# Kernel optimization log

Hardware: AMD Instinct MI355X
Metric: run time of the kernel (lower is better)

## Reference

```python
import jax, jax.numpy as jnp
import numpy as np

# Spiking time schedule: B_n = (1+0.5)*X_n = 1500 per spiking layer (X_n=1000),
# chained via set_params: layer k has t_min = 1500*k, t_max = 1500*(k+1).
B_N = 1500.0


def _region_idx(H, W):
    # 0=center, 1=TL, 2=top, 3=TR, 4=right, 5=BR, 6=bottom, 7=BL, 8=left
    r = np.zeros((H, W), np.int32)
    r[0, :] = 2; r[-1, :] = 6; r[:, 0] = 8; r[:, -1] = 4
    r[0, 0] = 1; r[0, -1] = 3; r[-1, -1] = 5; r[-1, 0] = 7
    return jnp.asarray(r)


def _im2col3(x, t_min):
    # x: [B,H,W,C] -> patches [B,H,W,9*C]; 'same' pad with value t_min
    B, H, W, C = x.shape
    xp = jnp.pad(x, ((0, 0), (1, 1), (1, 1), (0, 0)), constant_values=t_min)
    cols = [xp[:, dy:dy + H, dx:dx + W, :] for dy in range(3) for dx in range(3)]
    return jnp.concatenate(cols, axis=-1)


def _spiking_conv(x, Wk, D, t_min, t_max):
    # ti = (tj - t_min) @ W + (t_max - t_min - D_region) + t_min, clamped at t_max
    p = _im2col3(x, t_min)                       # [B,H,W,9C]
    lin = jnp.einsum('bhwk,kf->bhwf', p - t_min, Wk)
    Dmap = D[_region_idx(x.shape[1], x.shape[2])]  # [H,W,F] border-aware thresholds
    return jnp.minimum(lin + (t_max - Dmap), t_max)


def _spiking_dense(x, Wk, D, t_min, t_max):
    return jnp.minimum((x - t_min) @ Wk + (t_max - D), t_max)


def _pool2(x):
    B, H, W, C = x.shape
    return x.reshape(B, H // 2, 2, W // 2, 2, C).max(axis=(2, 4))


def _forward(x, Wc1, Dc1, Wc2, Dc2, Wc3, Dc3, Wc4, Dc4, Wd1, Dd1, Wout, Dout):
    x = _spiking_conv(x, Wc1, Dc1, 0.0, 1500.0)
    x = _spiking_conv(x, Wc2, Dc2, 1500.0, 3000.0)
    x = _pool2(x)
    x = _spiking_conv(x, Wc3, Dc3, 3000.0, 4500.0)
    x = _spiking_conv(x, Wc4, Dc4, 4500.0, 6000.0)
    x = _pool2(x)
    x = x.reshape(x.shape[0], -1)                 # [B, 16*16*128]
    x = _spiking_dense(x, Wd1, Dd1, 6000.0, 7500.0)
    # output layer: alpha*(t_min - t_min_prev) + (t_min - tj)@W == D_i + (t_min - tj)@W
    return Dout + (7500.0 - x) @ Wout


def setup_inputs() -> dict:
    key = jax.random.key(0)
    ks = jax.random.split(key, 14)
    B, H, C0 = 32, 64, 1

    def w(k, fan_in, fan_out):
        return (jax.random.normal(k, (fan_in, fan_out), jnp.float32)
                / np.float32(np.sqrt(fan_in)))

    def d(k, shape):
        return jax.random.uniform(k, shape, jnp.float32) * 10.0

    return {
        'x': jax.random.uniform(ks[0], (B, H, H, C0), jnp.float32),
        'Wc1': w(ks[1], 9 * C0, 64),    'Dc1': d(ks[2], (9, 64)),
        'Wc2': w(ks[3], 9 * 64, 64),    'Dc2': d(ks[4], (9, 64)),
        'Wc3': w(ks[5], 9 * 64, 128),   'Dc3': d(ks[6], (9, 128)),
        'Wc4': w(ks[7], 9 * 128, 128),  'Dc4': d(ks[8], (9, 128)),
        'Wd1': w(ks[9], 16 * 16 * 128, 256), 'Dd1': d(ks[10], (256,)),
        'Wout': w(ks[11], 256, 10),     'Dout': d(ks[12], (10,)),
    }


def reference(x, Wc1, Dc1, Wc2, Dc2, Wc3, Dc3, Wc4, Dc4, Wd1, Dd1, Wout, Dout):
    return _forward(x, Wc1, Dc1, Wc2, Dc2, Wc3, Dc3, Wc4, Dc4, Wd1, Dd1, Wout, Dout)
```

## Files before the change

kernel.cpp:

```cpp
#include <hip/hip_runtime.h>
#include <hip/hip_bf16.h>

#define DEVINL __device__ __forceinline__

typedef __attribute__((ext_vector_type(8)))  short short8;
typedef __attribute__((ext_vector_type(4)))  float float4v;

DEVINL float bf2f(unsigned short u) { return __uint_as_float(((unsigned)u) << 16); }
DEVINL unsigned short f2bf(float f) {
  unsigned u = __float_as_uint(f);
  unsigned r = u + 0x7FFFu + ((u >> 16) & 1u);
  return (unsigned short)(r >> 16);
}
DEVINL unsigned f2bf_u(float f) { return (unsigned)f2bf(f); }

DEVINL int region_of(int h, int w, int n) {
  if (h == 0)     return (w == 0) ? 1 : ((w == n-1) ? 3 : 2);
  if (h == n-1)   return (w == 0) ? 7 : ((w == n-1) ? 5 : 6);
  return (w == 0) ? 8 : ((w == n-1) ? 4 : 0);
}

__global__ void sentinel_k(float* out, float v) {
  int t = blockIdx.x*64 + threadIdx.x;
  if (t < 320) out[t] = v;
}

__global__ void wtrans_all(const float* __restrict__ W1, const float* __restrict__ W2,
                           const float* __restrict__ W3, const float* __restrict__ W4,
                           unsigned short* __restrict__ T1, unsigned short* __restrict__ T2,
                           unsigned short* __restrict__ T3, unsigned short* __restrict__ T4)
{
  int y = blockIdx.y;
  int i = blockIdx.x*256 + threadIdx.x;
  if (y == 3) {
    if (i >= 256) return;
    int lane = i & 63, nt = i >> 6;
    int lm = lane & 15, q = lane >> 4;
    int f = nt*16 + lm;
    unsigned short v[8] = {0,0,0,0,0,0,0,0};
    if ((q & 1) == 0) {
      #pragma unroll
      for (int j = 0; j < 8; j++) v[j] = f2bf(W1[j*64 + f]);
    } else {
      v[0] = f2bf(W1[8*64 + f]);
    }
    ushort4* qq = (ushort4*)&T1[(size_t)i * 8];
    qq[0] = make_ushort4(v[0], v[1], v[2], v[3]);
    qq[1] = make_ushort4(v[4], v[5], v[6], v[7]);
    return;
  }
  const float* W = (y == 0) ? W2 : (y == 1) ? W3 : W4;
  unsigned short* T = (y == 0) ? T2 : (y == 1) ? T3 : T4;
  int Ksteps = (y == 2) ? 36 : 18;
  int NT = (y == 0) ? 4 : 8;
  int F  = (y == 0) ? 64 : 128;
  if (i >= Ksteps*NT*64) return;
  int lane = i & 63, nt = (i >> 6) % NT, kstep = i / (64*NT);
  int f = nt*16 + (lane & 15);
  int kbase = kstep*32 + (lane >> 4)*8;
  unsigned short v[8];
  #pragma unroll
  for (int j = 0; j < 8; j++) v[j] = f2bf(W[(kbase + j)*F + f]);
  ushort4* q = (ushort4*)&T[(size_t)i * 8];
  q[0] = make_ushort4(v[0], v[1], v[2], v[3]);
  q[1] = make_ushort4(v[4], v[5], v[6], v[7]);
}

__global__ __launch_bounds__(256, 4) void conv12_k(const float* __restrict__ x,
    const unsigned short* __restrict__ Wt1, const float* __restrict__ Df1,
    const unsigned short* __restrict__ Wt, const float* __restrict__ Df2,
    unsigned short* __restrict__ out)
{
  constexpr int Cpad = 72;
  __shared__ __align__(16) unsigned short u[4*66*Cpad];
  __shared__ float xs[6][66];

  int b = blockIdx.y, hp = blockIdx.x, t = threadIdx.x;
  int h0 = hp * 2;

  for (int idx = t; idx < 6*66; idx += 256) {
    int r = idx / 66, wc = idx % 66;
    int hh = h0 - 2 + r, w = wc - 1;
    float v = 0.f;
    if (hh >= 0 && hh < 64 && w >= 0 && w < 64) v = x[(b*64 + hh)*64 + w];
    xs[r][wc] = v;
  }
  {
    int r = t >> 6, c = (t >> 5) & 1, f2 = (t & 31) * 2;
    *(unsigned*)&u[(r*66 + (c ? 65 : 0))*Cpad + f2] = 0u;
  }
  __syncthreads();

  int lane = t & 63, wave = t >> 6;
  int quad = lane >> 4, lm = lane & 15;
  union ABu { float4 f4; short8 v; };
  union AW  { unsigned w32[4]; short8 v; };

  {
    short8 b1[4];
    #pragma unroll
    for (int nt = 0; nt < 4; nt++) {
      ABu tmp;
      tmp.f4 = *(const float4*)&Wt1[(size_t)((nt*64) + lane)*8];
      b1[nt] = tmp.v;
    }
    int wl = wave*16 + lm;
    bool fullq = ((quad & 1) == 0);
    bool hiq   = (quad < 2);

    for (int r = 0; r < 4; r++) {
      int hh = h0 - 1 + r;
      if (hh >= 0 && hh < 64) {
        float v[9];
        #pragma unroll
        for (int k = 0; k < 9; k++) v[k] = xs[r + k/3][wl + k%3];
        unsigned hb[9], lb[9];
        #pragma unroll
        for (int k = 0; k < 9; k++) {
          hb[k] = f2bf_u(v[k]);
          lb[k] = f2bf_u(v[k] - bf2f((unsigned short)hb[k]));
        }
        unsigned Hp[4], Lp[4];
        #pragma unroll
        for (int j = 0; j < 4; j++) {
          Hp[j] = hb[2*j] | (hb[2*j+1] << 16);
          Lp[j] = lb[2*j] | (lb[2*j+1] << 16);
        }
        AW a;
        a.w32[0] = fullq ? (hiq ? Hp[0] : Lp[0]) : (hiq ? hb[8] : lb[8]);
        a.w32[1] = fullq ? (hiq ? Hp[1] : Lp[1]) : 0u;
        a.w32[2] = fullq ? (hiq ? Hp[2] : Lp[2]) : 0u;
        a.w32[3] = fullq ? (hiq ? Hp[3] : Lp[3]) : 0u;

        float4v acc1[4];
        #pragma unroll
        for (int nt = 0; nt < 4; nt++)
          acc1[nt] = __builtin_amdgcn_mfma_f32_16x16x32_bf16(a.v, b1[nt],
                       (float4v){0.f,0.f,0.f,0.f}, 0, 0, 0);

        #pragma unroll
        for (int nt = 0; nt < 4; nt++) {
          int f = nt*16 + lm;
          #pragma unroll
          for (int reg = 0; reg < 4; reg++) {
            int w = wave*16 + quad*4 + reg;
            float val = fminf(acc1[nt][reg] - Df1[region_of(hh, w, 64)*64 + f], 0.f);
            u[(r*66 + (w+1))*Cpad + f] = f2bf(val);
          }
        }
      } else {
        #pragma unroll
        for (int nt = 0; nt < 4; nt++)
          #pragma unroll
          for (int reg = 0; reg < 4; reg++)
            u[(r*66 + (wave*16 + quad*4 + reg + 1))*Cpad + nt*16 + lm] = 0;
      }
    }
  }
  __syncthreads();

  int wm = wave >> 1, wn = wave & 1;

  float4v acc[2][2][2];
  #pragma unroll
  for (int hi = 0; hi < 2; hi++)
    #pragma unroll
    for (int m = 0; m < 2; m++)
      #pragma unroll
      for (int n = 0; n < 2; n++)
        acc[hi][m][n] = (float4v){0.f, 0.f, 0.f, 0.f};

  #pragma unroll
  for (int dy = 0; dy < 3; dy++)
  #pragma unroll
  for (int dx = 0; dx < 3; dx++)
  #pragma unroll
  for (int c0 = 0; c0 < 64; c0 += 32) {
    int kstep = (dy*3 + dx)*2 + (c0 >> 5);
    ABu bfr[2];
    #pragma unroll
    for (int n = 0; n < 2; n++)
      bfr[n].f4 = *(const float4*)&Wt[(size_t)((kstep*4 + wn*2 + n)*64 + lane)*8];
    #pragma unroll
    for (int hi = 0; hi < 2; hi++) {
      ABu afr[2];
      #pragma unroll
      for (int m = 0; m < 2; m++)
        afr[m].f4 = *(const float4*)&u[((hi+dy)*66 + ((wm*2 + m)*16 + lm + dx))*Cpad + c0 + quad*8];
      #pragma unroll
      for (int n = 0; n < 2; n++)
        #pragma unroll
        for (int m = 0; m < 2; m++)
          acc[hi][m][n] = __builtin_amdgcn_mfma_f32_16x16x32_bf16(afr[m].v, bfr[n].v, acc[hi][m][n], 0, 0, 0);
    }
  }

  #pragma unroll
  for (int m = 0; m < 2; m++)
    #pragma unroll
    for (int n = 0; n < 2; n++) {
      int mm = wm*2 + m;
      int f = (wn*2 + n)*16 + lm;
      #pragma unroll
      for (int rp = 0; rp < 2; rp++) {
        float mx = -1e30f;
        #pragma unroll
        for (int hi = 0; hi < 2; hi++)
          #pragma unroll
          for (int rr = 0; rr < 2; rr++) {
            int h = h0 + hi, w = mm*16 + quad*4 + 2*rp + rr;
            float v = fminf(acc[hi][m][n][2*rp+rr] - Df2[region_of(h, w, 64)*64 + f], 0.f);
            mx = fmaxf(mx, v);
          }
        int wp = mm*8 + quad*2 + rp;
        out[(((size_t)b*32 + hp)*32 + wp)*64 + f] = f2bf(mx);
      }
    }
}

template<int C, int F, int N, bool POOL, int FS, int MINW>
__global__ __launch_bounds__(256, MINW) void conv_mfma(
    const unsigned short* __restrict__ U, const unsigned short* __restrict__ Wt,
    const float* __restrict__ Df, unsigned short* __restrict__ out)
{
  constexpr int RC   = POOL ? 2 : 1;
  constexpr int ROWS = RC + 2;
  constexpr int Cpad = C + 8;
  constexpr int NT = F / 16;
  constexpr int MT = N / 16;
  constexpr int NTE = NT / FS;
  constexpr int MW = MT;
  constexpr int NW = NTE / 4;

  __shared__ __align__(16) unsigned short lds[ROWS*(N+2)*Cpad];

  int bx = blockIdx.x, b = blockIdx.y, t = threadIdx.x;
  int hp = bx / FS, fs = bx % FS;
  int h0 = hp * RC;

  const int stage16 = ROWS*(N+2)*(C/8);
  #pragma unroll 4
  for (int i = t; i < stage16; i += 256) {
    int c8 = i % (C/8), wc = (i/(C/8)) % (N+2), r = i/((C/8)*(N+2));
    int hh = h0 - 1 + r, w = wc - 1;
    float4 v = make_float4(0.f,0.f,0.f,0.f);
    if (hh >= 0 && hh < N && w >= 0 && w < N)
      v = *(const float4*)&U[(((size_t)b*N + hh)*N + w)*C + c8*8];
    *(float4*)&lds[(r*(N+2) + wc)*Cpad + c8*8] = v;
  }
  __syncthreads();

  int lane = t & 63, wave = t >> 6;
  int wn = wave;
  int quad = lane >> 4, lm = lane & 15;

  union ABu { float4 f4; short8 v; };

  float4v acc[RC][MW][NW];
  #pragma unroll
  for (int hi = 0; hi < RC; hi++)
    #pragma unroll
    for (int m = 0; m < MW; m++)
      #pragma unroll
      for (int n = 0; n < NW; n++)
        acc[hi][m][n] = (float4v){0.f, 0.f, 0.f, 0.f};

  #pragma unroll
  for (int dy = 0; dy < 3; dy++)
  #pragma unroll
  for (int dx = 0; dx < 3; dx++)
  #pragma unroll
  for (int c0 = 0; c0 < C; c0 += 32) {
    int kstep = (dy*3 + dx)*(C/32) + (c0 >> 5);
    ABu bfr[NW];
    #pragma unroll
    for (int n = 0; n < NW; n++)
      bfr[n].f4 = *(const float4*)&Wt[(size_t)((kstep*NT + fs*NTE + wn*NW + n)*64 + lane)*8];
    #pragma unroll
    for (int hi = 0; hi < RC; hi++) {
      ABu afr[MW];
      #pragma unroll
      for (int m = 0; m < MW; m++)
        afr[m].f4 = *(const float4*)&lds[((hi+dy)*(N+2) + (m*16 + lm + dx))*Cpad + c0 + quad*8];
      #pragma unroll
      for (int n = 0; n < NW; n++)
        #pragma unroll
        for (int m = 0; m < MW; m++)
          acc[hi][m][n] = __builtin_amdgcn_mfma_f32_16x16x32_bf16(afr[m].v, bfr[n].v, acc[hi][m][n], 0, 0, 0);
    }
  }

  if constexpr (POOL) {
    constexpr int M2 = N/2;
    #pragma unroll
    for (int m = 0; m < MW; m++)
      #pragma unroll
      for (int n = 0; n < NW; n++) {
        int f = (fs*NTE + wn*NW + n)*16 + lm;
        #pragma unroll
        for (int rp = 0; rp < 2; rp++) {
          float mx = -1e30f;
          #pragma unroll
          for (int hi = 0; hi < 2; hi++)
            #pragma unroll
            for (int rr = 0; rr < 2; rr++) {
              int h = h0 + hi, w = m*16 + quad*4 + 2*rp + rr;
              float v = fminf(acc[hi][m][n][2*rp+rr] - Df[region_of(h, w, N)*F + f], 0.f);
              mx = fmaxf(mx, v);
            }
          int wp = m*8 + quad*2 + rp;
          out[(((size_t)b*M2 + hp)*M2 + wp)*F + f] = f2bf(mx);
        }
      }
  } else {
    int h = h0;
    #pragma unroll
    for (int m = 0; m < MW; m++)
      #pragma unroll
      for (int n = 0; n < NW; n++) {
        int f = (fs*NTE + wn*NW + n)*16 + lm;
        #pragma unroll
        for (int r = 0; r < 4; r++) {
          int w = m*16 + quad*4 + r;
          int reg = region_of(h, w, N);
          float v = fminf(acc[0][m][n][r] - Df[reg*F + f], 0.f);
          out[(((size_t)b*N + h)*N + w)*F + f] = f2bf(v);
        }
      }
  }
}

__global__ __launch_bounds__(256, 2) void conv4_k(
    const unsigned short* __restrict__ U, const unsigned short* __restrict__ Wt,
    const float* __restrict__ Df, unsigned short* __restrict__ out)
{
  constexpr int C = 128, Cpad = 136, N = 32;
  __shared__ __align__(16) unsigned short lds[3*34*Cpad];

  int b = blockIdx.y, hp = blockIdx.x, t = threadIdx.x;
  int h0 = hp * 2;

  const int stage16 = 3*34*(C/8);
  #pragma unroll 4
  for (int i = t; i < stage16; i += 256) {
    int c8 = i % 16, wc = (i/16) % 34, r = i/(16*34);
    int hh = h0 - 1 + r, w = wc - 1;
    float4 v = make_float4(0.f,0.f,0.f,0.f);
    if (hh >= 0 && hh < N && w >= 0 && w < N)
      v = *(const float4*)&U[(((size_t)b*N + hh)*N + w)*C + c8*8];
    *(float4*)&lds[(r*34 + wc)*Cpad + c8*8] = v;
  }
  __syncthreads();

  int lane = t & 63, wave = t >> 6;
  int wn = wave, quad = lane >> 4, lm = lane & 15;
  union ABu { float4 f4; short8 v; };

  float4v acc[2][2][2];
  #pragma unroll
  for (int hi = 0; hi < 2; hi++)
    #pragma unroll
    for (int m = 0; m < 2; m++)
      #pragma unroll
      for (int n = 0; n < 2; n++)
        acc[hi][m][n] = (float4v){0.f, 0.f, 0.f, 0.f};

  #pragma unroll
  for (int dy = 0; dy < 3; dy++)
  #pragma unroll
  for (int dx = 0; dx < 3; dx++)
  #pragma unroll
  for (int c0 = 0; c0 < C; c0 += 32) {
    int kstep = (dy*3 + dx)*4 + (c0 >> 5);
    ABu bfr[2];
    #pragma unroll
    for (int n = 0; n < 2; n++)
      bfr[n].f4 = *(const float4*)&Wt[(size_t)((kstep*8 + wn*2 + n)*64 + lane)*8];

    ABu afr0[2];
    #pragma unroll
    for (int m = 0; m < 2; m++)
      afr0[m].f4 = *(const float4*)&lds[(dy*34 + (m*16 + lm + dx))*Cpad + c0 + quad*8];

    ABu afr1[2];
    {
      int h1 = h0 + dy;
      #pragma unroll
      for (int m = 0; m < 2; m++) {
        int wo = m*16 + lm + dx - 1;
        float4 av = make_float4(0.f,0.f,0.f,0.f);
        if (h1 < N && wo >= 0 && wo < N)
          av = *(const float4*)&U[(((size_t)b*N + h1)*N + wo)*C + c0 + quad*8];
        afr1[m].f4 = av;
      }
    }

    #pragma unroll
    for (int n = 0; n < 2; n++)
      #pragma unroll
      for (int m = 0; m < 2; m++)
        acc[0][m][n] = __builtin_amdgcn_mfma_f32_16x16x32_bf16(afr0[m].v, bfr[n].v, acc[0][m][n], 0, 0, 0);
    #pragma unroll
    for (int n = 0; n < 2; n++)
      #pragma unroll
      for (int m = 0; m < 2; m++)
        acc[1][m][n] = __builtin_amdgcn_mfma_f32_16x16x32_bf16(afr1[m].v, bfr[n].v, acc[1][m][n], 0, 0, 0);
  }

  #pragma unroll
  for (int m = 0; m < 2; m++)
    #pragma unroll
    for (int n = 0; n < 2; n++) {
      int f = (wn*2 + n)*16 + lm;
      #pragma unroll
      for (int rp = 0; rp < 2; rp++) {
        float mx = -1e30f;
        #pragma unroll
        for (int hi = 0; hi < 2; hi++)
          #pragma unroll
          for (int rr = 0; rr < 2; rr++) {
            int h = h0 + hi, w = m*16 + quad*4 + 2*rp + rr;
            float v = fminf(acc[hi][m][n][2*rp+rr] - Df[region_of(h, w, N)*128 + f], 0.f);
            mx = fmaxf(mx, v);
          }
        int wp = m*8 + quad*2 + rp;
        out[(((size_t)b*16 + hp)*16 + wp)*128 + f] = f2bf(mx);
      }
    }
}

__global__ __launch_bounds__(256) void dense_k(const unsigned short* __restrict__ act,
    const float* __restrict__ W, float* __restrict__ part)
{
  int blk = blockIdx.x, t = threadIdx.x;
  int kblk = blk >> 1, fh = blk & 1;
  int k0 = kblk * 128;
  __shared__ float a[128][36];
  for (int idx = t; idx < 32*128; idx += 256) {
    int bb = idx >> 7, kc = idx & 127;
    a[kc][bb] = bf2f(act[(size_t)bb*32768 + k0 + kc]);
  }
  __syncthreads();
  int f0 = fh*128 + (t & 31)*4, b0 = (t >> 5)*4;
  float acc[4][4] = {};
  #pragma unroll 8
  for (int kc = 0; kc < 128; kc++) {
    float4 wv = *(const float4*)&W[(size_t)(k0 + kc)*256 + f0];
    float4 av = *(const float4*)&a[kc][b0];
    const float* avp = (const float*)&av;
    #pragma unroll
    for (int bb = 0; bb < 4; bb++) {
      float avx = avp[bb];
      acc[bb][0] += avx * wv.x;
      acc[bb][1] += avx * wv.y;
      acc[bb][2] += avx * wv.z;
      acc[bb][3] += avx * wv.w;
    }
  }
  #pragma unroll
  for (int bb = 0; bb < 4; bb++) {
    float4 v = make_float4(acc[bb][0], acc[bb][1], acc[bb][2], acc[bb][3]);
    *(float4*)&part[(size_t)kblk*8192 + (b0+bb)*256 + f0] = v;
  }
}

__global__ __launch_bounds__(1024) void redfin_k(const float* __restrict__ part,
    const float* __restrict__ Dd, const float* __restrict__ Wo,
    const float* __restrict__ Do, float* __restrict__ out)
{
  int b = blockIdx.x, t = threadIdx.x;
  int f = t & 255, kq = t >> 8;
  float s = 0.f;
  #pragma unroll 16
  for (int blk = kq*64; blk < kq*64 + 64; blk++)
    s += part[(size_t)blk*8192 + b*256 + f];
  __shared__ float red[4][256];
  red[kq][f] = s;
  __syncthreads();
  __shared__ float ud[256];
  if (t < 256) {
    float v = red[0][t] + red[1][t] + red[2][t] + red[3][t];
    ud[t] = fminf(v - Dd[t], 0.f);
  }
  __syncthreads();
  int lane = t & 63, wave = t >> 6;
  if (wave < 4) {
    for (int o = wave; o < 10; o += 4) {
      float acc = 0.f;
      #pragma unroll
      for (int j = 0; j < 4; j++) {
        int ff = j*64 + lane;
        acc += ud[ff] * Wo[ff*10 + o];
      }
      #pragma unroll
      for (int off = 32; off; off >>= 1) acc += __shfl_down(acc, off, 64);
      if (lane == 0) out[b*10 + o] = Do[o] - acc;
    }
  }
}

extern "C" void kernel_launch(void* const* d_in, const int* in_sizes, int n_in,
                              void* d_out, int out_size, void* d_ws, size_t ws_size,
                              hipStream_t stream)
{
  float* outp = (float*)d_out;

  if (n_in != 13) { sentinel_k<<<5, 64, 0, stream>>>(outp, 200.f); return; }
  const int exp_sz[13] = {131072, 576, 576, 36864, 576, 73728, 1152,
                          147456, 1152, 8388608, 256, 2560, 10};
  for (int i = 0; i < 13; i++)
    if (in_sizes[i] != exp_sz[i]) {
      sentinel_k<<<5, 64, 0, stream>>>(outp, 1000.f + 100.f*i); return;
    }
  if (ws_size < (37u << 20)) { sentinel_k<<<5, 64, 0, stream>>>(outp, 500.f); return; }

  char* wsb = (char*)d_ws;
  const float* x    = (const float*)d_in[0];
  const float* Wc1  = (const float*)d_in[1];
  const float* Dc1  = (const float*)d_in[2];
  const float* Wc2  = (const float*)d_in[3];
  const float* Dc2  = (const float*)d_in[4];
  const float* Wc3  = (const float*)d_in[5];
  const float* Dc3  = (const float*)d_in[6];
  const float* Wc4  = (const float*)d_in[7];
  const float* Dc4  = (const float*)d_in[8];
  const float* Wd1  = (const float*)d_in[9];
  const float* Dd1  = (const float*)d_in[10];
  const float* Wout = (const float*)d_in[11];
  const float* Dout = (const float*)d_in[12];

  unsigned short* Wt2 = (unsigned short*)(wsb + (1u << 20));
  unsigned short* Wt3 = (unsigned short*)(wsb + (1u << 20) + 262144);
  unsigned short* Wt4 = (unsigned short*)(wsb + (1u << 20) + 524288);
  unsigned short* Wt1 = (unsigned short*)(wsb + (1u << 20) + 921600);
  unsigned short* P2  = (unsigned short*)(wsb + (19u << 20));
  unsigned short* U3  = (unsigned short*)(wsb + (2u  << 20));
  unsigned short* P4  = (unsigned short*)(wsb + (25u << 20));
  float* part         = (float*)(wsb + (2u  << 20));

  wtrans_all<<<dim3(72, 4), 256, 0, stream>>>(Wc1, Wc2, Wc3, Wc4, Wt1, Wt2, Wt3, Wt4);
  conv12_k<<<dim3(32, 32), 256, 0, stream>>>(x, Wt1, Dc1, Wt2, Dc2, P2);
  conv_mfma<64, 128, 32, false, 1, 2><<<dim3(32, 32), 256, 0, stream>>>(P2, Wt3, Dc3, U3);
  conv4_k<<<dim3(16, 32), 256, 0, stream>>>(U3, Wt4, Dc4, P4);
  dense_k<<<512, 256, 0, stream>>>(P4, Wd1, part);
  redfin_k<<<32, 1024, 0, stream>>>(part, Dd1, Wout, Dout, outp);
}
```

Baseline: 162.5 us.

## Split conv4 tiles by width halves and stage all rows in LDS

conv4 blocks now cover two output rows and half the width (16 columns), so twice as many blocks are launched. All four input rows are staged in LDS, replacing the direct global loads previously used for the second output row. Each wave holds fewer accumulators and the launch bound asks for 4 blocks per SM for more occupancy. The trade-off is more redundant halo staging and more weight-fragment loads per output.

```diff
diff --git a/kernel.cpp b/kernel.cpp
--- a/kernel.cpp
+++ b/kernel.cpp
@@ -330,40 +330,39 @@
   }
 }
 
-__global__ __launch_bounds__(256, 2) void conv4_k(
+__global__ __launch_bounds__(256, 4) void conv4_k(
     const unsigned short* __restrict__ U, const unsigned short* __restrict__ Wt,
     const float* __restrict__ Df, unsigned short* __restrict__ out)
 {
   constexpr int C = 128, Cpad = 136, N = 32;
-  __shared__ __align__(16) unsigned short lds[3*34*Cpad];
-
-  int b = blockIdx.y, hp = blockIdx.x, t = threadIdx.x;
-  int h0 = hp * 2;
-
-  const int stage16 = 3*34*(C/8);
+  __shared__ __align__(16) unsigned short lds[4*18*Cpad];
+
+  int bx = blockIdx.x, b = blockIdx.y, t = threadIdx.x;
+  int hp = bx >> 1, ms = bx & 1;
+  int h0 = hp * 2, w0 = ms * 16;
+
+  const int stage16 = 4*18*16;
   #pragma unroll 4
   for (int i = t; i < stage16; i += 256) {
-    int c8 = i % 16, wc = (i/16) % 34, r = i/(16*34);
-    int hh = h0 - 1 + r, w = wc - 1;
+    int c8 = i & 15, wc = (i >> 4) % 18, r = i / (16*18);
+    int hh = h0 - 1 + r, w = w0 - 1 + wc;
     float4 v = make_float4(0.f,0.f,0.f,0.f);
     if (hh >= 0 && hh < N && w >= 0 && w < N)
       v = *(const float4*)&U[(((size_t)b*N + hh)*N + w)*C + c8*8];
-    *(float4*)&lds[(r*34 + wc)*Cpad + c8*8] = v;
+    *(float4*)&lds[(r*18 + wc)*Cpad + c8*8] = v;
   }
   __syncthreads();
 
   int lane = t & 63, wave = t >> 6;
-  int wn = wave, quad = lane >> 4, lm = lane & 15;
+  int quad = lane >> 4, lm = lane & 15;
   union ABu { float4 f4; short8 v; };
 
-  float4v acc[2][2][2];
+  float4v acc[2][2];
   #pragma unroll
   for (int hi = 0; hi < 2; hi++)
     #pragma unroll
-    for (int m = 0; m < 2; m++)
-      #pragma unroll
-      for (int n = 0; n < 2; n++)
-        acc[hi][m][n] = (float4v){0.f, 0.f, 0.f, 0.f};
+    for (int n = 0; n < 2; n++)
+      acc[hi][n] = (float4v){0.f, 0.f, 0.f, 0.f};
 
   #pragma unroll
   for (int dy = 0; dy < 3; dy++)
@@ -375,58 +374,36 @@
     ABu bfr[2];
     #pragma unroll
     for (int n = 0; n < 2; n++)
-      bfr[n].f4 = *(const float4*)&Wt[(size_t)((kstep*8 + wn*2 + n)*64 + lane)*8];
-
-    ABu afr0[2];
-    #pragma unroll
-    for (int m = 0; m < 2; m++)
-      afr0[m].f4 = *(const float4*)&lds[(dy*34 + (m*16 + lm + dx))*Cpad + c0 + quad*8];
-
-    ABu afr1[2];
-    {
-      int h1 = h0 + dy;
-      #pragma unroll
-      for (int m = 0; m < 2; m++) {
-        int wo = m*16 + lm + dx - 1;
-        float4 av = make_float4(0.f,0.f,0.f,0.f);
-        if (h1 < N && wo >= 0 && wo < N)
-          av = *(const float4*)&U[(((size_t)b*N + h1)*N + wo)*C + c0 + quad*8];
-        afr1[m].f4 = av;
-      }
-    }
-
-    #pragma unroll
-    for (int n = 0; n < 2; n++)
-      #pragma unroll
-      for (int m = 0; m < 2; m++)
-        acc[0][m][n] = __builtin_amdgcn_mfma_f32_16x16x32_bf16(afr0[m].v, bfr[n].v, acc[0][m][n], 0, 0, 0);
-    #pragma unroll
-    for (int n = 0; n < 2; n++)
-      #pragma unroll
-      for (int m = 0; m < 2; m++)
-        acc[1][m][n] = __builtin_amdgcn_mfma_f32_16x16x32_bf16(afr1[m].v, bfr[n].v, acc[1][m][n], 0, 0, 0);
-  }
-
-  #pragma unroll
-  for (int m = 0; m < 2; m++)
-    #pragma unroll
-    for (int n = 0; n < 2; n++) {
-      int f = (wn*2 + n)*16 + lm;
-      #pragma unroll
-      for (int rp = 0; rp < 2; rp++) {
-        float mx = -1e30f;
-        #pragma unroll
-        for (int hi = 0; hi < 2; hi++)
-          #pragma unroll
-          for (int rr = 0; rr < 2; rr++) {
-            int h = h0 + hi, w = m*16 + quad*4 + 2*rp + rr;
-            float v = fminf(acc[hi][m][n][2*rp+rr] - Df[region_of(h, w, N)*128 + f], 0.f);
-            mx = fmaxf(mx, v);
-          }
-        int wp = m*8 + quad*2 + rp;
-        out[(((size_t)b*16 + hp)*16 + wp)*128 + f] = f2bf(mx);
-      }
-    }
+      bfr[n].f4 = *(const float4*)&Wt[(size_t)((kstep*8 + wave*2 + n)*64 + lane)*8];
+    ABu afr[2];
+    #pragma unroll
+    for (int hi = 0; hi < 2; hi++)
+      afr[hi].f4 = *(const float4*)&lds[((hi+dy)*18 + (lm + dx))*Cpad + c0 + quad*8];
+    #pragma unroll
+    for (int hi = 0; hi < 2; hi++)
+      #pragma unroll
+      for (int n = 0; n < 2; n++)
+        acc[hi][n] = __builtin_amdgcn_mfma_f32_16x16x32_bf16(afr[hi].v, bfr[n].v, acc[hi][n], 0, 0, 0);
+  }
+
+  #pragma unroll
+  for (int n = 0; n < 2; n++) {
+    int f = (wave*2 + n)*16 + lm;
+    #pragma unroll
+    for (int rp = 0; rp < 2; rp++) {
+      float mx = -1e30f;
+      #pragma unroll
+      for (int hi = 0; hi < 2; hi++)
+        #pragma unroll
+        for (int rr = 0; rr < 2; rr++) {
+          int h = h0 + hi, w = w0 + quad*4 + 2*rp + rr;
+          float v = fminf(acc[hi][n][2*rp+rr] - Df[region_of(h, w, N)*128 + f], 0.f);
+          mx = fmaxf(mx, v);
+        }
+      int wp = ms*8 + quad*2 + rp;
+      out[(((size_t)b*16 + hp)*16 + wp)*128 + f] = f2bf(mx);
+    }
+  }
 }
 
 __global__ __launch_bounds__(256) void dense_k(const unsigned short* __restrict__ act,
@@ -541,7 +518,7 @@
   wtrans_all<<<dim3(72, 4), 256, 0, stream>>>(Wc1, Wc2, Wc3, Wc4, Wt1, Wt2, Wt3, Wt4);
   conv12_k<<<dim3(32, 32), 256, 0, stream>>>(x, Wt1, Dc1, Wt2, Dc2, P2);
   conv_mfma<64, 128, 32, false, 1, 2><<<dim3(32, 32), 256, 0, stream>>>(P2, Wt3, Dc3, U3);
-  conv4_k<<<dim3(16, 32), 256, 0, stream>>>(U3, Wt4, Dc4, P4);
+  conv4_k<<<dim3(32, 32), 256, 0, stream>>>(U3, Wt4, Dc4, P4);
   dense_k<<<512, 256, 0, stream>>>(P4, Wd1, part);
   redfin_k<<<32, 1024, 0, stream>>>(part, Dd1, Wout, Dout, outp);
 }
```

After: 154.8 us. 1.05x faster.
